# Optimization experiments

Hardware: AMD Instinct MI355X
Metric: run time of the kernel (lower is better)

## Reference

```python
import jax, jax.numpy as jnp
import numpy as np

N = 50000      # nodes
E = 800000     # edges
IN = 128       # in_channels
HID = 64       # hidden_channels
HEADS = 4
OUT = 2        # out_channels


def setup_inputs() -> dict:
    key = jax.random.key(0)
    ks = jax.random.split(key, 14)
    p = lambda k, shape: 0.1 * jax.random.normal(k, shape, dtype=jnp.float32)
    x = jax.random.normal(ks[0], (N, IN), dtype=jnp.float32)
    edge_index = jax.random.randint(ks[1], (2, E), 0, N, dtype=jnp.int64)
    return {
        'x': x, 'edge_index': edge_index,
        'W1': p(ks[2], (IN, HEADS * HID)), 'a_src1': p(ks[3], (HEADS, HID)),
        'a_dst1': p(ks[4], (HEADS, HID)), 'b1': p(ks[5], (HEADS * HID,)),
        'W2': p(ks[6], (HEADS * HID, HID)), 'a_src2': p(ks[7], (1, HID)),
        'a_dst2': p(ks[8], (1, HID)), 'b2': p(ks[9], (HID,)),
        'Wm1': p(ks[10], (2 * HID, HID)), 'bm1': p(ks[11], (HID,)),
        'Wm2': p(ks[12], (HID, OUT)), 'bm2': p(ks[13], (OUT,)),
    }


def _gat_conv(x, src, dst, W, a_src, a_dst, b, heads, out_c, concat):
    """PyG GATConv (eval mode): linear -> per-edge leakyrelu score ->
    segment softmax over destination -> scatter-sum aggregation."""
    n = x.shape[0]
    h = (x @ W).reshape(n, heads, out_c)                 # [N,H,C]
    s_src = jnp.einsum('nhc,hc->nh', h, a_src)           # [N,H]
    s_dst = jnp.einsum('nhc,hc->nh', h, a_dst)           # [N,H]
    e = jax.nn.leaky_relu(s_src[src] + s_dst[dst], 0.2)  # [E,H]
    m = jax.ops.segment_max(e, dst, num_segments=n)      # per-dst max (self-loops => no empty segs)
    ex = jnp.exp(e - m[dst])
    denom = jax.ops.segment_sum(ex, dst, num_segments=n)
    alpha = ex / (denom[dst] + 1e-16)                    # [E,H]
    out = jax.ops.segment_sum(h[src] * alpha[:, :, None], dst, num_segments=n)  # [N,H,C]
    if concat:
        return out.reshape(n, heads * out_c) + b
    return out.mean(axis=1) + b


def reference(x, edge_index, W1, a_src1, a_dst1, b1, W2, a_src2, a_dst2, b2,
              Wm1, bm1, Wm2, bm2):
    n = x.shape[0]
    loop = jnp.arange(n, dtype=edge_index.dtype)
    # GATConv add_self_loops=True (default)
    src = jnp.concatenate([edge_index[0], loop])
    dst = jnp.concatenate([edge_index[1], loop])
    h1 = jax.nn.relu(_gat_conv(x, src, dst, W1, a_src1, a_dst1, b1, HEADS, HID, True))
    h2 = _gat_conv(h1, src, dst, W2, a_src2, a_dst2, b2, 1, HID, False)   # [N,HID]
    parents, children = edge_index[0], edge_index[1]
    ef = jnp.concatenate([h2[parents], h2[children]], axis=1)             # [E,2*HID]
    return jax.nn.relu(ef @ Wm1 + bm1) @ Wm2 + bm2                        # [E,OUT]
```

## Files before the change

kernel.cpp:

```cpp
#include <hip/hip_runtime.h>
#include <hip/hip_fp16.h>

#define NN 50000
#define EE 800000
#define ENE (EE + NN)

typedef _Float16 f16;
typedef __attribute__((ext_vector_type(8))) _Float16 f16x8;
typedef __attribute__((ext_vector_type(4))) _Float16 f16x4;
typedef __attribute__((ext_vector_type(4))) float f32x4;


__global__ __launch_bounds__(256)
void deg_kernel(const int* __restrict__ ei, int* __restrict__ deg) {
    int i = blockIdx.x * 256 + threadIdx.x;
    if (i >= ENE) return;
    int d = (i < EE) ? ei[EE + i] : (i - EE);
    atomicAdd(&deg[d], 1);
}

__global__ __launch_bounds__(1024)
void scan1_kernel(const int* __restrict__ deg, int* __restrict__ offs,
                  int* __restrict__ bsum) {
    __shared__ int s[1024];
    int t = threadIdx.x;
    int i = blockIdx.x * 1024 + t;
    int v = (i < NN) ? deg[i] : 0;
    s[t] = v;
    __syncthreads();
    for (int off = 1; off < 1024; off <<= 1) {
        int a = (t >= off) ? s[t - off] : 0;
        __syncthreads();
        s[t] += a;
        __syncthreads();
    }
    if (i < NN) offs[i] = s[t] - v;
    if (t == 1023) bsum[blockIdx.x] = s[1023];
}

__global__ __launch_bounds__(64)
void scan2_kernel(const int* __restrict__ bsum, int* __restrict__ bpre, int nb) {
    if (threadIdx.x == 0) {
        int run = 0;
        for (int b = 0; b < nb; ++b) { bpre[b] = run; run += bsum[b]; }
    }
}

__global__ __launch_bounds__(256)
void scan3_kernel(int* __restrict__ offs, const int* __restrict__ bpre) {
    int i = blockIdx.x * 256 + threadIdx.x;
    if (i >= NN) return;
    offs[i] += bpre[i >> 10];
}

__global__ __launch_bounds__(256)
void scatter_kernel(const int* __restrict__ ei, int* __restrict__ offs,
                    int* __restrict__ csr_src, int* __restrict__ csr_dst) {
    int i = blockIdx.x * 256 + threadIdx.x;
    if (i >= ENE) return;
    int d, s;
    if (i < EE) { s = ei[i]; d = ei[EE + i]; }
    else        { s = i - EE; d = i - EE; }
    int p = atomicAdd(&offs[d], 1);
    csr_src[p] = s;
    csr_dst[p] = d;
}


__global__ __launch_bounds__(256)
void cast_w_kernel(const float* __restrict__ W1, const float* __restrict__ W2,
                   const float* __restrict__ Wm1, f16* __restrict__ W1t,
                   f16* __restrict__ W2t, f16* __restrict__ Wmt) {
    int idx = blockIdx.x * 256 + threadIdx.x;
    if (idx < 32768) {
        int j = idx >> 7, k = idx & 127;
        W1t[idx] = (f16)W1[k * 256 + j];
    } else if (idx < 49152) {
        int i = idx - 32768;
        int j = i >> 8, k = i & 255;
        W2t[i] = (f16)W2[k * 64 + j];
    } else if (idx < 57344) {
        int i = idx - 49152;
        int j = i >> 6, k = i & 63;
        float v = (j < 64) ? Wm1[k * 64 + j] : Wm1[(64 + k) * 64 + (j - 64)];
        Wmt[i] = (f16)v;
    }
}


template<int K, int NOUT, int NWR, int NWC, int PERM, int AF32, int SCORES>
__global__ __launch_bounds__(256)
void mfma_gemm(const void* __restrict__ Avoid, const f16* __restrict__ Bt,
               f16* __restrict__ Yh, const float* __restrict__ a_src,
               const float* __restrict__ a_dst, float* __restrict__ ss,
               float* __restrict__ sd, int nrows) {
    constexpr int BROWS = NWR * 16;
    constexpr int LDP = NOUT + 8;
    __shared__ f16 lds[BROWS * LDP];
    const int tid = threadIdx.x;
    const int wid = tid >> 6, lane = tid & 63;
    const int wr = wid / NWC, wc = wid % NWC;
    const int lm = lane & 15, lk = lane >> 4;
    const int row0 = blockIdx.x * BROWS + wr * 16;
    const int col0 = wc * 64;

    const float* A32 = (const float*)Avoid;
    const f16*   A16 = (const f16*)Avoid;

    int arow = row0 + lm;
    if (arow >= nrows) arow = nrows - 1;

    f32x4 acc[4] = {};
#pragma unroll
    for (int ks = 0; ks < K / 32; ++ks) {
        f16x8 af;
        if (AF32) {
            float4 v0 = *(const float4*)&A32[(size_t)arow * K + ks * 32 + lk * 8];
            float4 v1 = *(const float4*)&A32[(size_t)arow * K + ks * 32 + lk * 8 + 4];
            af = f16x8{(f16)v0.x, (f16)v0.y, (f16)v0.z, (f16)v0.w,
                       (f16)v1.x, (f16)v1.y, (f16)v1.z, (f16)v1.w};
        } else {
            af = *(const f16x8*)(A16 + (size_t)arow * K + ks * 32 + lk * 8);
        }
#pragma unroll
        for (int ct = 0; ct < 4; ++ct) {
            const f16* bptr = Bt + (size_t)(col0 + ct * 16 + lm) * K + ks * 32 + lk * 8;
            f16x8 bf = *(const f16x8*)bptr;
            acc[ct] = __builtin_amdgcn_mfma_f32_16x16x32_f16(af, bf, acc[ct], 0, 0, 0);
        }
    }

#pragma unroll
    for (int ct = 0; ct < 4; ++ct) {
#pragma unroll
        for (int r = 0; r < 4; ++r) {
            int lrow = wr * 16 + lk * 4 + r;
            int j = col0 + ct * 16 + lm;
            int jj = PERM ? ((j & 63) * 4 + (j >> 6)) : j;
            lds[lrow * LDP + jj] = (f16)acc[ct][r];
        }
    }
    __syncthreads();

    constexpr int CHUNKS = NOUT / 8;
    for (int idx = tid; idx < BROWS * CHUNKS; idx += 256) {
        int lrow = idx / CHUNKS, ch = idx % CHUNKS;
        int grow = blockIdx.x * BROWS + lrow;
        if (grow < nrows) {
            f16x8 v = *(const f16x8*)&lds[lrow * LDP + ch * 8];
            *(f16x8*)&Yh[(size_t)grow * NOUT + ch * 8] = v;
        }
    }

    if (SCORES == 1) {
        int rloc = wid * 4 + (lane >> 4);
        int ci = lane & 15;
        float ps[4] = {}, pd[4] = {};
#pragma unroll
        for (int cc = 0; cc < 4; ++cc) {
            int c = ci + cc * 16;
            f16x4 hv = *(const f16x4*)&lds[rloc * LDP + c * 4];
#pragma unroll
            for (int h = 0; h < 4; ++h) {
                float f = (float)hv[h];
                ps[h] += f * a_src[h * 64 + c];
                pd[h] += f * a_dst[h * 64 + c];
            }
        }
#pragma unroll
        for (int m = 1; m < 16; m <<= 1) {
#pragma unroll
            for (int h = 0; h < 4; ++h) {
                ps[h] += __shfl_xor(ps[h], m);
                pd[h] += __shfl_xor(pd[h], m);
            }
        }
        if (ci == 0) {
            int grow = blockIdx.x * BROWS + rloc;
            if (grow < nrows) {
                *(float4*)&ss[grow * 4] = make_float4(ps[0], ps[1], ps[2], ps[3]);
                *(float4*)&sd[grow * 4] = make_float4(pd[0], pd[1], pd[2], pd[3]);
            }
        }
    } else if (SCORES == 2) {
        int rloc = wid * 16 + (lane >> 2);
        int cg = lane & 3;
        float ps = 0.f, pd = 0.f;
#pragma unroll
        for (int b = 0; b < 2; ++b) {
            f16x8 hv = *(const f16x8*)&lds[rloc * LDP + cg * 16 + b * 8];
#pragma unroll
            for (int u = 0; u < 8; ++u) {
                int c = cg * 16 + b * 8 + u;
                float f = (float)hv[u];
                ps += f * a_src[c];
                pd += f * a_dst[c];
            }
        }
        ps += __shfl_xor(ps, 1); ps += __shfl_xor(ps, 2);
        pd += __shfl_xor(pd, 1); pd += __shfl_xor(pd, 2);
        if (cg == 0) {
            int grow = blockIdx.x * BROWS + rloc;
            if (grow < nrows) { ss[grow] = ps; sd[grow] = pd; }
        }
    }
}


__global__ __launch_bounds__(256)
void p1_kernel(const int* __restrict__ csr_src, const int* __restrict__ csr_dst,
               const float* __restrict__ ss, const float* __restrict__ sd,
               float4* __restrict__ p1) {
    int j = blockIdx.x * 256 + threadIdx.x;
    if (j >= ENE) return;
    int s = csr_src[j], d = csr_dst[j];
    float4 a = *(const float4*)&ss[s * 4];
    float4 b = *(const float4*)&sd[d * 4];
    float e0 = a.x + b.x; e0 = e0 > 0.f ? e0 : 0.2f * e0;
    float e1 = a.y + b.y; e1 = e1 > 0.f ? e1 : 0.2f * e1;
    float e2 = a.z + b.z; e2 = e2 > 0.f ? e2 : 0.2f * e2;
    float e3 = a.w + b.w; e3 = e3 > 0.f ? e3 : 0.2f * e3;
    p1[j] = make_float4(__expf(e0), __expf(e1), __expf(e2), __expf(e3));
}

__global__ __launch_bounds__(256)
void p2_kernel(const int* __restrict__ csr_src, const int* __restrict__ csr_dst,
               const float* __restrict__ ss, const float* __restrict__ sd,
               float* __restrict__ p2) {
    int j = blockIdx.x * 256 + threadIdx.x;
    if (j >= ENE) return;
    float e = ss[csr_src[j]] + sd[csr_dst[j]];
    e = e > 0.f ? e : 0.2f * e;
    p2[j] = __expf(e);
}


__global__ __launch_bounds__(256)
void agg1_kernel(const int* __restrict__ offs, const int* __restrict__ csr_src,
                 const float4* __restrict__ p1, const f16* __restrict__ h1h,
                 const float* __restrict__ b1, f16* __restrict__ h1half) {
    int lane = threadIdx.x & 63;
    int n = blockIdx.x * 4 + (threadIdx.x >> 6);
    if (n >= NN) return;
    int beg = (n == 0) ? 0 : offs[n - 1];
    int end = offs[n];
    float den0 = 0.f, den1 = 0.f, den2 = 0.f, den3 = 0.f;
    float ac0 = 0.f, ac1 = 0.f, ac2 = 0.f, ac3 = 0.f;
    int j = beg;
    for (; j + 8 <= end; j += 8) {
        int s[8];
#pragma unroll
        for (int u = 0; u < 8; ++u) s[u] = csr_src[j + u];
        float4 q[8];
#pragma unroll
        for (int u = 0; u < 8; ++u) q[u] = p1[j + u];
        f16x4 hv[8];
#pragma unroll
        for (int u = 0; u < 8; ++u)
            hv[u] = *(const f16x4*)&h1h[(size_t)s[u] * 256 + lane * 4];
#pragma unroll
        for (int u = 0; u < 8; ++u) {
            den0 += q[u].x; den1 += q[u].y; den2 += q[u].z; den3 += q[u].w;
            ac0 += q[u].x * (float)hv[u][0];
            ac1 += q[u].y * (float)hv[u][1];
            ac2 += q[u].z * (float)hv[u][2];
            ac3 += q[u].w * (float)hv[u][3];
        }
    }
    for (; j < end; ++j) {
        int s = csr_src[j];
        float4 pv = p1[j];
        f16x4 hv = *(const f16x4*)&h1h[(size_t)s * 256 + lane * 4];
        den0 += pv.x; den1 += pv.y; den2 += pv.z; den3 += pv.w;
        ac0 += pv.x * (float)hv[0];
        ac1 += pv.y * (float)hv[1];
        ac2 += pv.z * (float)hv[2];
        ac3 += pv.w * (float)hv[3];
    }
    float r0 = ac0 / (den0 + 1e-16f) + b1[lane];
    float r1 = ac1 / (den1 + 1e-16f) + b1[64 + lane];
    float r2 = ac2 / (den2 + 1e-16f) + b1[128 + lane];
    float r3 = ac3 / (den3 + 1e-16f) + b1[192 + lane];
    f16* orow = &h1half[(size_t)n * 256];
    orow[lane]       = (f16)(r0 > 0.f ? r0 : 0.f);
    orow[64 + lane]  = (f16)(r1 > 0.f ? r1 : 0.f);
    orow[128 + lane] = (f16)(r2 > 0.f ? r2 : 0.f);
    orow[192 + lane] = (f16)(r3 > 0.f ? r3 : 0.f);
}

__global__ __launch_bounds__(256)
void agg2_kernel(const int* __restrict__ offs, const int* __restrict__ csr_src,
                 const float* __restrict__ p2, const f16* __restrict__ h2linh,
                 const float* __restrict__ b2, f16* __restrict__ h2half) {
    int lane = threadIdx.x & 63;
    int n = blockIdx.x * 4 + (threadIdx.x >> 6);
    if (n >= NN) return;
    int beg = (n == 0) ? 0 : offs[n - 1];
    int end = offs[n];
    float den = 0.f, acc = 0.f;
    int j = beg;
    for (; j + 8 <= end; j += 8) {
        int s[8];
#pragma unroll
        for (int u = 0; u < 8; ++u) s[u] = csr_src[j + u];
        float q[8];
#pragma unroll
        for (int u = 0; u < 8; ++u) q[u] = p2[j + u];
        float v[8];
#pragma unroll
        for (int u = 0; u < 8; ++u)
            v[u] = (float)h2linh[(size_t)s[u] * 64 + lane];
#pragma unroll
        for (int u = 0; u < 8; ++u) {
            den += q[u];
            acc += q[u] * v[u];
        }
    }
    for (; j < end; ++j) {
        int s = csr_src[j];
        float p = p2[j];
        den += p;
        acc += p * (float)h2linh[(size_t)s * 64 + lane];
    }
    h2half[(size_t)n * 64 + lane] = (f16)(acc / (den + 1e-16f) + b2[lane]);
}


__global__ __launch_bounds__(256)
void edge_kernel(const int* __restrict__ ei, const f16* __restrict__ gh,
                 const float* __restrict__ bm1, const float* __restrict__ Wm2,
                 const float* __restrict__ bm2, float* __restrict__ out) {
    int l = threadIdx.x & 15;
    int eid = blockIdx.x * 16 + (threadIdx.x >> 4);
    if (eid >= EE) return;
    int p = ei[eid];
    int c = ei[EE + eid];
    f16x4 av = *(const f16x4*)&gh[(size_t)p * 128 + l * 4];
    f16x4 bv = *(const f16x4*)&gh[(size_t)c * 128 + 64 + l * 4];
    float4 bb = *(const float4*)&bm1[l * 4];
    float zx = (float)av[0] + (float)bv[0] + bb.x; zx = zx > 0.f ? zx : 0.f;
    float zy = (float)av[1] + (float)bv[1] + bb.y; zy = zy > 0.f ? zy : 0.f;
    float zz = (float)av[2] + (float)bv[2] + bb.z; zz = zz > 0.f ? zz : 0.f;
    float zw = (float)av[3] + (float)bv[3] + bb.w; zw = zw > 0.f ? zw : 0.f;
    float4 w01 = *(const float4*)&Wm2[l * 8];
    float4 w23 = *(const float4*)&Wm2[l * 8 + 4];
    float o0 = zx * w01.x + zy * w01.z + zz * w23.x + zw * w23.z;
    float o1 = zx * w01.y + zy * w01.w + zz * w23.y + zw * w23.w;
#pragma unroll
    for (int m = 1; m < 16; m <<= 1) {
        o0 += __shfl_xor(o0, m);
        o1 += __shfl_xor(o1, m);
    }
    if (l == 0)
        *(float2*)&out[(size_t)eid * 2] = make_float2(o0 + bm2[0], o1 + bm2[1]);
}


extern "C" void kernel_launch(void* const* d_in, const int* in_sizes, int n_in,
                              void* d_out, int out_size, void* d_ws, size_t ws_size,
                              hipStream_t stream) {
    const float* x      = (const float*)d_in[0];
    const int*   ei     = (const int*)d_in[1];
    const float* W1     = (const float*)d_in[2];
    const float* a_src1 = (const float*)d_in[3];
    const float* a_dst1 = (const float*)d_in[4];
    const float* b1     = (const float*)d_in[5];
    const float* W2     = (const float*)d_in[6];
    const float* a_src2 = (const float*)d_in[7];
    const float* a_dst2 = (const float*)d_in[8];
    const float* b2     = (const float*)d_in[9];
    const float* Wm1    = (const float*)d_in[10];
    const float* bm1    = (const float*)d_in[11];
    const float* Wm2    = (const float*)d_in[12];
    const float* bm2    = (const float*)d_in[13];
    float* out = (float*)d_out;

    char* ws = (char*)d_ws;
    size_t off = 0;
    auto alloc = [&](size_t bytes) -> void* {
        void* p = ws + off;
        off += (bytes + 255) & ~(size_t)255;
        return p;
    };
    int*    deg     = (int*)alloc((size_t)NN * 4);
    int*    offs    = (int*)alloc((size_t)NN * 4);
    int*    bsum    = (int*)alloc(64 * 4);
    int*    bpre    = (int*)alloc(64 * 4);
    int*    csr_src = (int*)alloc((size_t)ENE * 4);
    int*    csr_dst = (int*)alloc((size_t)ENE * 4);
    float*  ss1     = (float*)alloc((size_t)NN * 4 * 4);
    float*  sd1     = (float*)alloc((size_t)NN * 4 * 4);
    float*  ss2     = (float*)alloc((size_t)NN * 4);
    float*  sd2     = (float*)alloc((size_t)NN * 4);
    float4* p1      = (float4*)alloc((size_t)ENE * 16);
    float*  p2      = (float*)alloc((size_t)ENE * 4);
    f16*    W1t     = (f16*)alloc((size_t)256 * 128 * 2);
    f16*    W2t     = (f16*)alloc((size_t)64 * 256 * 2);
    f16*    Wmt     = (f16*)alloc((size_t)128 * 64 * 2);
    f16*    h1h     = (f16*)alloc((size_t)NN * 256 * 2);
    f16*    h1half  = (f16*)alloc((size_t)NN * 256 * 2);
    f16*    h2linh  = (f16*)alloc((size_t)NN * 64 * 2);
    f16*    h2half  = (f16*)alloc((size_t)NN * 64 * 2);
    f16*    gh      = (f16*)alloc((size_t)NN * 128 * 2);
    if (off > ws_size) return;

    const int nbScan  = (NN + 1023) / 1024;
    const int gEdges  = (ENE + 255) / 256;
    const int gNodes4 = (NN + 3) / 4;
    const int gEdge16 = (EE + 15) / 16;

    cast_w_kernel<<<(57344 + 255) / 256, 256, 0, stream>>>(W1, W2, Wm1, W1t, W2t, Wmt);

    hipMemsetAsync(deg, 0, (size_t)NN * 4, stream);
    deg_kernel<<<gEdges, 256, 0, stream>>>(ei, deg);
    scan1_kernel<<<nbScan, 1024, 0, stream>>>(deg, offs, bsum);
    scan2_kernel<<<1, 64, 0, stream>>>(bsum, bpre, nbScan);
    scan3_kernel<<<(NN + 255) / 256, 256, 0, stream>>>(offs, bpre);
    scatter_kernel<<<gEdges, 256, 0, stream>>>(ei, offs, csr_src, csr_dst);

    mfma_gemm<128, 256, 1, 4, 1, 1, 1><<<NN / 16, 256, 0, stream>>>(
        x, W1t, h1h, a_src1, a_dst1, ss1, sd1, NN);
    p1_kernel<<<gEdges, 256, 0, stream>>>(csr_src, csr_dst, ss1, sd1, p1);
    agg1_kernel<<<gNodes4, 256, 0, stream>>>(offs, csr_src, p1, h1h, b1, h1half);

    mfma_gemm<256, 64, 4, 1, 0, 0, 2><<<(NN + 63) / 64, 256, 0, stream>>>(
        h1half, W2t, h2linh, a_src2, a_dst2, ss2, sd2, NN);
    p2_kernel<<<gEdges, 256, 0, stream>>>(csr_src, csr_dst, ss2, sd2, p2);
    agg2_kernel<<<gNodes4, 256, 0, stream>>>(offs, csr_src, p2, h2linh, b2, h2half);

    mfma_gemm<64, 128, 2, 2, 0, 0, 0><<<(NN + 31) / 32, 256, 0, stream>>>(
        h2half, Wmt, gh, nullptr, nullptr, nullptr, nullptr, NN);
    edge_kernel<<<gEdge16, 256, 0, stream>>>(ei, gh, bm1, Wm2, bm2, out);
}
```

Before: 427.4 us.

## Fuse edge-score computation into CSR scatter and split aggregation across half-waves

The CSR scatter kernel now also computes the layer-1 exponentiated attention scores and writes them to the CSR slot, so the separate p1 pass is gone. To allow this, the scatter moves after the first GEMM. Both aggregation kernels now split each node's edge list between two half-wavefronts, each doing wider per-lane loads (f16x8 / f16x2), and combine the halves with cross-lane shuffles. This cuts a launch and a pass over the edges and increases memory-level parallelism in the gathers. In exchange the scatter's writes are random and the GEMM can no longer overlap with CSR construction.

```diff
diff --git a/kernel.cpp b/kernel.cpp
--- a/kernel.cpp
+++ b/kernel.cpp
@@ -8,6 +8,7 @@
 typedef _Float16 f16;
 typedef __attribute__((ext_vector_type(8))) _Float16 f16x8;
 typedef __attribute__((ext_vector_type(4))) _Float16 f16x4;
+typedef __attribute__((ext_vector_type(2))) _Float16 f16x2;
 typedef __attribute__((ext_vector_type(4))) float f32x4;
 
 
@@ -54,16 +55,25 @@
 }
 
 __global__ __launch_bounds__(256)
-void scatter_kernel(const int* __restrict__ ei, int* __restrict__ offs,
-                    int* __restrict__ csr_src, int* __restrict__ csr_dst) {
+void scatter_p1_kernel(const int* __restrict__ ei, int* __restrict__ offs,
+                       int* __restrict__ csr_src, int* __restrict__ csr_dst,
+                       const float* __restrict__ ss, const float* __restrict__ sd,
+                       float4* __restrict__ p1) {
     int i = blockIdx.x * 256 + threadIdx.x;
     if (i >= ENE) return;
     int d, s;
     if (i < EE) { s = ei[i]; d = ei[EE + i]; }
     else        { s = i - EE; d = i - EE; }
-    int p = atomicAdd(&offs[d], 1);
-    csr_src[p] = s;
-    csr_dst[p] = d;
+    int slot = atomicAdd(&offs[d], 1);
+    csr_src[slot] = s;
+    csr_dst[slot] = d;
+    float4 a = *(const float4*)&ss[s * 4];
+    float4 b = *(const float4*)&sd[d * 4];
+    float e0 = a.x + b.x; e0 = e0 > 0.f ? e0 : 0.2f * e0;
+    float e1 = a.y + b.y; e1 = e1 > 0.f ? e1 : 0.2f * e1;
+    float e2 = a.z + b.z; e2 = e2 > 0.f ? e2 : 0.2f * e2;
+    float e3 = a.w + b.w; e3 = e3 > 0.f ? e3 : 0.2f * e3;
+    p1[slot] = make_float4(__expf(e0), __expf(e1), __expf(e2), __expf(e3));
 }
 
 
@@ -208,22 +218,6 @@
 
 
 __global__ __launch_bounds__(256)
-void p1_kernel(const int* __restrict__ csr_src, const int* __restrict__ csr_dst,
-               const float* __restrict__ ss, const float* __restrict__ sd,
-               float4* __restrict__ p1) {
-    int j = blockIdx.x * 256 + threadIdx.x;
-    if (j >= ENE) return;
-    int s = csr_src[j], d = csr_dst[j];
-    float4 a = *(const float4*)&ss[s * 4];
-    float4 b = *(const float4*)&sd[d * 4];
-    float e0 = a.x + b.x; e0 = e0 > 0.f ? e0 : 0.2f * e0;
-    float e1 = a.y + b.y; e1 = e1 > 0.f ? e1 : 0.2f * e1;
-    float e2 = a.z + b.z; e2 = e2 > 0.f ? e2 : 0.2f * e2;
-    float e3 = a.w + b.w; e3 = e3 > 0.f ? e3 : 0.2f * e3;
-    p1[j] = make_float4(__expf(e0), __expf(e1), __expf(e2), __expf(e3));
-}
-
-__global__ __launch_bounds__(256)
 void p2_kernel(const int* __restrict__ csr_src, const int* __restrict__ csr_dst,
                const float* __restrict__ ss, const float* __restrict__ sd,
                float* __restrict__ p2) {
@@ -240,52 +234,94 @@
                  const float4* __restrict__ p1, const f16* __restrict__ h1h,
                  const float* __restrict__ b1, f16* __restrict__ h1half) {
     int lane = threadIdx.x & 63;
+    int hw = lane >> 5;
+    int l = lane & 31;
     int n = blockIdx.x * 4 + (threadIdx.x >> 6);
     if (n >= NN) return;
     int beg = (n == 0) ? 0 : offs[n - 1];
     int end = offs[n];
+
     float den0 = 0.f, den1 = 0.f, den2 = 0.f, den3 = 0.f;
-    float ac0 = 0.f, ac1 = 0.f, ac2 = 0.f, ac3 = 0.f;
-    int j = beg;
-    for (; j + 8 <= end; j += 8) {
-        int s[8];
-#pragma unroll
-        for (int u = 0; u < 8; ++u) s[u] = csr_src[j + u];
-        float4 q[8];
-#pragma unroll
-        for (int u = 0; u < 8; ++u) q[u] = p1[j + u];
-        f16x4 hv[8];
-#pragma unroll
-        for (int u = 0; u < 8; ++u)
-            hv[u] = *(const f16x4*)&h1h[(size_t)s[u] * 256 + lane * 4];
-#pragma unroll
-        for (int u = 0; u < 8; ++u) {
-            den0 += q[u].x; den1 += q[u].y; den2 += q[u].z; den3 += q[u].w;
-            ac0 += q[u].x * (float)hv[u][0];
-            ac1 += q[u].y * (float)hv[u][1];
-            ac2 += q[u].z * (float)hv[u][2];
-            ac3 += q[u].w * (float)hv[u][3];
-        }
-    }
-    for (; j < end; ++j) {
-        int s = csr_src[j];
-        float4 pv = p1[j];
-        f16x4 hv = *(const f16x4*)&h1h[(size_t)s * 256 + lane * 4];
-        den0 += pv.x; den1 += pv.y; den2 += pv.z; den3 += pv.w;
-        ac0 += pv.x * (float)hv[0];
-        ac1 += pv.y * (float)hv[1];
-        ac2 += pv.z * (float)hv[2];
-        ac3 += pv.w * (float)hv[3];
-    }
-    float r0 = ac0 / (den0 + 1e-16f) + b1[lane];
-    float r1 = ac1 / (den1 + 1e-16f) + b1[64 + lane];
-    float r2 = ac2 / (den2 + 1e-16f) + b1[128 + lane];
-    float r3 = ac3 / (den3 + 1e-16f) + b1[192 + lane];
-    f16* orow = &h1half[(size_t)n * 256];
-    orow[lane]       = (f16)(r0 > 0.f ? r0 : 0.f);
-    orow[64 + lane]  = (f16)(r1 > 0.f ? r1 : 0.f);
-    orow[128 + lane] = (f16)(r2 > 0.f ? r2 : 0.f);
-    orow[192 + lane] = (f16)(r3 > 0.f ? r3 : 0.f);
+    float aA0 = 0.f, aA1 = 0.f, aA2 = 0.f, aA3 = 0.f;
+    float aB0 = 0.f, aB1 = 0.f, aB2 = 0.f, aB3 = 0.f;
+    int j = beg + hw;
+
+#define AGG1_BODY(JJ)                                                          \
+    {                                                                          \
+        int s_ = csr_src[JJ];                                                  \
+        float4 q_ = p1[JJ];                                                    \
+        f16x8 hv_ = *(const f16x8*)&h1h[(size_t)s_ * 256 + l * 8];             \
+        den0 += q_.x; den1 += q_.y; den2 += q_.z; den3 += q_.w;                \
+        aA0 += q_.x * (float)hv_[0]; aB0 += q_.x * (float)hv_[4];              \
+        aA1 += q_.y * (float)hv_[1]; aB1 += q_.y * (float)hv_[5];              \
+        aA2 += q_.z * (float)hv_[2]; aB2 += q_.z * (float)hv_[6];              \
+        aA3 += q_.w * (float)hv_[3]; aB3 += q_.w * (float)hv_[7];              \
+    }
+
+    for (; j + 6 < end; j += 8) {
+        int s0 = csr_src[j + 0];
+        int s1 = csr_src[j + 2];
+        int s2 = csr_src[j + 4];
+        int s3 = csr_src[j + 6];
+        float4 q0 = p1[j + 0];
+        float4 q1 = p1[j + 2];
+        float4 q2 = p1[j + 4];
+        float4 q3 = p1[j + 6];
+        f16x8 h0 = *(const f16x8*)&h1h[(size_t)s0 * 256 + l * 8];
+        f16x8 h1v = *(const f16x8*)&h1h[(size_t)s1 * 256 + l * 8];
+        f16x8 h2v = *(const f16x8*)&h1h[(size_t)s2 * 256 + l * 8];
+        f16x8 h3v = *(const f16x8*)&h1h[(size_t)s3 * 256 + l * 8];
+        den0 += (q0.x + q1.x) + (q2.x + q3.x);
+        den1 += (q0.y + q1.y) + (q2.y + q3.y);
+        den2 += (q0.z + q1.z) + (q2.z + q3.z);
+        den3 += (q0.w + q1.w) + (q2.w + q3.w);
+        aA0 += q0.x * (float)h0[0] + q1.x * (float)h1v[0]
+             + q2.x * (float)h2v[0] + q3.x * (float)h3v[0];
+        aB0 += q0.x * (float)h0[4] + q1.x * (float)h1v[4]
+             + q2.x * (float)h2v[4] + q3.x * (float)h3v[4];
+        aA1 += q0.y * (float)h0[1] + q1.y * (float)h1v[1]
+             + q2.y * (float)h2v[1] + q3.y * (float)h3v[1];
+        aB1 += q0.y * (float)h0[5] + q1.y * (float)h1v[5]
+             + q2.y * (float)h2v[5] + q3.y * (float)h3v[5];
+        aA2 += q0.z * (float)h0[2] + q1.z * (float)h1v[2]
+             + q2.z * (float)h2v[2] + q3.z * (float)h3v[2];
+        aB2 += q0.z * (float)h0[6] + q1.z * (float)h1v[6]
+             + q2.z * (float)h2v[6] + q3.z * (float)h3v[6];
+        aA3 += q0.w * (float)h0[3] + q1.w * (float)h1v[3]
+             + q2.w * (float)h2v[3] + q3.w * (float)h3v[3];
+        aB3 += q0.w * (float)h0[7] + q1.w * (float)h1v[7]
+             + q2.w * (float)h2v[7] + q3.w * (float)h3v[7];
+    }
+    for (; j < end; j += 2) AGG1_BODY(j);
+#undef AGG1_BODY
+
+    den0 += __shfl_xor(den0, 32); den1 += __shfl_xor(den1, 32);
+    den2 += __shfl_xor(den2, 32); den3 += __shfl_xor(den3, 32);
+    aA0 += __shfl_xor(aA0, 32);   aB0 += __shfl_xor(aB0, 32);
+    aA1 += __shfl_xor(aA1, 32);   aB1 += __shfl_xor(aB1, 32);
+    aA2 += __shfl_xor(aA2, 32);   aB2 += __shfl_xor(aB2, 32);
+    aA3 += __shfl_xor(aA3, 32);   aB3 += __shfl_xor(aB3, 32);
+
+    if (hw == 0) {
+        f16* orow = &h1half[(size_t)n * 256];
+        float i0 = 1.f / (den0 + 1e-16f);
+        float i1 = 1.f / (den1 + 1e-16f);
+        float i2 = 1.f / (den2 + 1e-16f);
+        float i3 = 1.f / (den3 + 1e-16f);
+        float2 bb0 = *(const float2*)&b1[0 * 64 + 2 * l];
+        float2 bb1 = *(const float2*)&b1[1 * 64 + 2 * l];
+        float2 bb2 = *(const float2*)&b1[2 * 64 + 2 * l];
+        float2 bb3 = *(const float2*)&b1[3 * 64 + 2 * l];
+        float rA, rB;
+        rA = aA0 * i0 + bb0.x; rB = aB0 * i0 + bb0.y;
+        *(f16x2*)&orow[0 * 64 + 2 * l] = f16x2{(f16)(rA > 0.f ? rA : 0.f), (f16)(rB > 0.f ? rB : 0.f)};
+        rA = aA1 * i1 + bb1.x; rB = aB1 * i1 + bb1.y;
+        *(f16x2*)&orow[1 * 64 + 2 * l] = f16x2{(f16)(rA > 0.f ? rA : 0.f), (f16)(rB > 0.f ? rB : 0.f)};
+        rA = aA2 * i2 + bb2.x; rB = aB2 * i2 + bb2.y;
+        *(f16x2*)&orow[2 * 64 + 2 * l] = f16x2{(f16)(rA > 0.f ? rA : 0.f), (f16)(rB > 0.f ? rB : 0.f)};
+        rA = aA3 * i3 + bb3.x; rB = aB3 * i3 + bb3.y;
+        *(f16x2*)&orow[3 * 64 + 2 * l] = f16x2{(f16)(rA > 0.f ? rA : 0.f), (f16)(rB > 0.f ? rB : 0.f)};
+    }
 }
 
 __global__ __launch_bounds__(256)
@@ -293,36 +329,53 @@
                  const float* __restrict__ p2, const f16* __restrict__ h2linh,
                  const float* __restrict__ b2, f16* __restrict__ h2half) {
     int lane = threadIdx.x & 63;
+    int hw = lane >> 5;
+    int l = lane & 31;
     int n = blockIdx.x * 4 + (threadIdx.x >> 6);
     if (n >= NN) return;
     int beg = (n == 0) ? 0 : offs[n - 1];
     int end = offs[n];
-    float den = 0.f, acc = 0.f;
-    int j = beg;
-    for (; j + 8 <= end; j += 8) {
-        int s[8];
-#pragma unroll
-        for (int u = 0; u < 8; ++u) s[u] = csr_src[j + u];
-        float q[8];
-#pragma unroll
-        for (int u = 0; u < 8; ++u) q[u] = p2[j + u];
-        float v[8];
-#pragma unroll
-        for (int u = 0; u < 8; ++u)
-            v[u] = (float)h2linh[(size_t)s[u] * 64 + lane];
-#pragma unroll
-        for (int u = 0; u < 8; ++u) {
-            den += q[u];
-            acc += q[u] * v[u];
-        }
-    }
-    for (; j < end; ++j) {
+
+    float den = 0.f, aA = 0.f, aB = 0.f;
+    int j = beg + hw;
+    for (; j + 6 < end; j += 8) {
+        int s0 = csr_src[j + 0];
+        int s1 = csr_src[j + 2];
+        int s2 = csr_src[j + 4];
+        int s3 = csr_src[j + 6];
+        float q0 = p2[j + 0];
+        float q1 = p2[j + 2];
+        float q2 = p2[j + 4];
+        float q3 = p2[j + 6];
+        f16x2 v0 = *(const f16x2*)&h2linh[(size_t)s0 * 64 + l * 2];
+        f16x2 v1 = *(const f16x2*)&h2linh[(size_t)s1 * 64 + l * 2];
+        f16x2 v2 = *(const f16x2*)&h2linh[(size_t)s2 * 64 + l * 2];
+        f16x2 v3 = *(const f16x2*)&h2linh[(size_t)s3 * 64 + l * 2];
+        den += (q0 + q1) + (q2 + q3);
+        aA += q0 * (float)v0[0] + q1 * (float)v1[0]
+            + q2 * (float)v2[0] + q3 * (float)v3[0];
+        aB += q0 * (float)v0[1] + q1 * (float)v1[1]
+            + q2 * (float)v2[1] + q3 * (float)v3[1];
+    }
+    for (; j < end; j += 2) {
         int s = csr_src[j];
-        float p = p2[j];
-        den += p;
-        acc += p * (float)h2linh[(size_t)s * 64 + lane];
-    }
-    h2half[(size_t)n * 64 + lane] = (f16)(acc / (den + 1e-16f) + b2[lane]);
+        float q = p2[j];
+        f16x2 v = *(const f16x2*)&h2linh[(size_t)s * 64 + l * 2];
+        den += q;
+        aA += q * (float)v[0];
+        aB += q * (float)v[1];
+    }
+
+    den += __shfl_xor(den, 32);
+    aA  += __shfl_xor(aA, 32);
+    aB  += __shfl_xor(aB, 32);
+
+    if (hw == 0) {
+        float inv = 1.f / (den + 1e-16f);
+        float2 bb = *(const float2*)&b2[2 * l];
+        f16x2 o = f16x2{(f16)(aA * inv + bb.x), (f16)(aB * inv + bb.y)};
+        *(f16x2*)&h2half[(size_t)n * 64 + 2 * l] = o;
+    }
 }
 
 
@@ -416,11 +469,12 @@
     scan1_kernel<<<nbScan, 1024, 0, stream>>>(deg, offs, bsum);
     scan2_kernel<<<1, 64, 0, stream>>>(bsum, bpre, nbScan);
     scan3_kernel<<<(NN + 255) / 256, 256, 0, stream>>>(offs, bpre);
-    scatter_kernel<<<gEdges, 256, 0, stream>>>(ei, offs, csr_src, csr_dst);
 
     mfma_gemm<128, 256, 1, 4, 1, 1, 1><<<NN / 16, 256, 0, stream>>>(
         x, W1t, h1h, a_src1, a_dst1, ss1, sd1, NN);
-    p1_kernel<<<gEdges, 256, 0, stream>>>(csr_src, csr_dst, ss1, sd1, p1);
+
+    scatter_p1_kernel<<<gEdges, 256, 0, stream>>>(ei, offs, csr_src, csr_dst,
+                                                  ss1, sd1, p1);
     agg1_kernel<<<gNodes4, 256, 0, stream>>>(offs, csr_src, p1, h1h, b1, h1half);
 
     mfma_gemm<256, 64, 4, 1, 0, 0, 2><<<(NN + 63) / 64, 256, 0, stream>>>(
```

Measured after the change: 406.8 us. 1.05x faster.
